# Optimization experiments

Measured on AMD Instinct MI355X. Metric: run time of the kernel, lower is better.

Reference implementation:

```python
import jax, jax.numpy as jnp
from jax import lax
import numpy as np

NUM_GROUP = 512   # num_group from __init__
GROUP_SIZE = 64   # group_size; walk length = GROUP_SIZE - 1


def setup_inputs() -> dict:
    key = jax.random.key(0)
    k1, k2, k3, k4 = jax.random.split(key, 4)
    B, N, V = 8, 65536, 32768
    xyz = jax.random.normal(k1, (B, N, 3), jnp.float32)
    ring_1 = jax.random.randint(k2, (B, N, 3), 0, N).astype(jnp.int32)
    vertices = jax.random.normal(k3, (B, V, 3), jnp.float32)
    faces = jax.random.randint(k4, (B, N, 3), 0, V).astype(jnp.int32)
    return {"xyz": xyz, "ring_1": ring_1, "vertices": vertices, "faces": faces}


def fps(xyz, num_group):
    # iterative farthest point sampling, deterministic start at index 0
    B, N, _ = xyz.shape
    idx0 = jnp.zeros((B,), jnp.int32)
    dist0 = jnp.full((B, N), 1e10, xyz.dtype)

    def body(carry, _):
        dist, last = carry
        p = jax.vmap(lambda x, i: x[i])(xyz, last)            # [B,3]
        d = jnp.sum((xyz - p[:, None, :]) ** 2, -1)           # [B,N]
        dist = jnp.minimum(dist, d)
        nxt = jnp.argmax(dist, axis=1).astype(jnp.int32)
        return (dist, nxt), nxt

    (_, _), rest = lax.scan(body, (dist0, idx0), None, length=num_group - 1)
    return jnp.concatenate([idx0[None, :], rest], 0).T        # [B,G]


def random_walks(ring, centers, n_faces, seq_len, key):
    # vectorized visited-mask random walk over all (batch, center) pairs
    B, G = centers.shape
    keys = jax.random.split(key, B * G).reshape(B, G)

    def one(nbrs_b, f0, k):
        visited = jnp.zeros((n_faces + 1,), bool).at[n_faces].set(True).at[f0].set(True)

        def step(carry, kk):
            cur, vis = carry
            nb = nbrs_b[cur]                                   # [3] neighbor ids
            mask = ~vis[nb]
            ka, kb = jax.random.split(kk)
            scores = jnp.where(mask, jax.random.uniform(ka, (3,)), -1.0)
            pick = nb[jnp.argmax(scores)]                      # random unvisited nbr
            rnd = jax.random.randint(kb, (), 0, n_faces)       # jump fallback
            nxt = jnp.where(mask.any(), pick, rnd).astype(jnp.int32)
            return (nxt, vis.at[nxt].set(True)), nxt

        (_, _), seq = lax.scan(step, (f0.astype(jnp.int32), visited),
                               jax.random.split(k, seq_len))
        return jnp.concatenate([f0[None].astype(jnp.int32), seq])

    return jax.vmap(lambda nb, cs, ks: jax.vmap(lambda f0, kk: one(nb, f0, kk))(cs, ks))(
        ring, centers, keys)                                   # [B,G,seq_len+1]


def reference(xyz, ring_1, vertices, faces):
    B, N, _ = xyz.shape
    center_idx = fps(xyz, NUM_GROUP)                           # [B,G]
    center = jax.vmap(lambda p, i: p[i])(xyz, center_idx)      # [B,G,3]
    idx = random_walks(ring_1, center_idx, N, GROUP_SIZE - 1, jax.random.key(42))
    neighborhood = jax.vmap(lambda p, i: p[i])(xyz, idx)       # [B,G,M,3]
    neighborhood = neighborhood - center[:, :, None, :]
    return neighborhood, center, idx.astype(jnp.int64)
```

## Files before the change

kernel.cpp:

```cpp
#include <hip/hip_runtime.h>
#include <stdint.h>

#define BB 8
#define NN 65536
#define GG 512
#define MM 64
#define STEPS 63
#define NWALK (BB*GG)

#define FPT 256
#define FPK 32
#define PPT (NN/(FPK*FPT))
#define FPS_BLOCKS (BB*FPK)

typedef unsigned long long ull;

__device__ __forceinline__ uint32_t rotl32(uint32_t x, uint32_t r){ return (x<<r)|(x>>(32u-r)); }

__device__ __forceinline__ void tf2x32(uint32_t k0, uint32_t k1, uint32_t x0, uint32_t x1,
                                       uint32_t &o0, uint32_t &o1){
  const uint32_t ks2 = k0 ^ k1 ^ 0x1BD11BDAu;
  x0 += k0; x1 += k1;
#define TFR(r) { x0 += x1; x1 = rotl32(x1,(r)); x1 ^= x0; }
  TFR(13) TFR(15) TFR(26) TFR(6)
  x0 += k1;  x1 += ks2 + 1u;
  TFR(17) TFR(29) TFR(16) TFR(24)
  x0 += ks2; x1 += k0 + 2u;
  TFR(13) TFR(15) TFR(26) TFR(6)
  x0 += k0;  x1 += k1 + 3u;
  TFR(17) TFR(29) TFR(16) TFR(24)
  x0 += k1;  x1 += ks2 + 4u;
  TFR(13) TFR(15) TFR(26) TFR(6)
  x0 += ks2; x1 += k0 + 5u;
#undef TFR
  o0 = x0; o1 = x1;
}

__global__ void rng_init_kernel(uint4* __restrict__ rng,
                                ull* __restrict__ slots,
                                int* __restrict__ center_idx){
  int tid = blockIdx.x*blockDim.x + threadIdx.x;
  if (tid < 2*BB*FPK) slots[tid] = 0ull;
  if (tid < BB) center_idx[tid*GG] = 0;
  if (tid >= STEPS*NWALK) return;
  int step = tid / NWALK;
  int walk = tid - step*NWALK;
  uint32_t kj0,kj1,t0,t1,a0,a1,b0,b1,p0,p1,q0,q1,r0,r1,l0,l1;
  tf2x32(0u, 42u, 0u, (uint32_t)walk, kj0, kj1);
  tf2x32(kj0, kj1, 0u, (uint32_t)step, t0, t1);
  tf2x32(t0, t1, 0u, 0u, a0, a1);
  tf2x32(t0, t1, 0u, 1u, b0, b1);
  tf2x32(a0, a1, 0u, 0u, p0, p1);
  tf2x32(a0, a1, 0u, 1u, q0, q1);
  tf2x32(a0, a1, 0u, 2u, r0, r1);
  tf2x32(b0, b1, 0u, 1u, l0, l1);
  uint4 e;
  e.x = ((p0 ^ p1) >> 9) | 0x3f800000u;
  e.y = ((q0 ^ q1) >> 9) | 0x3f800000u;
  e.z = ((r0 ^ r1) >> 9) | 0x3f800000u;
  e.w = (l0 ^ l1) & 0xFFFFu;
  rng[tid] = e;
}

__global__ __launch_bounds__(FPT) void fps_kernel(const float* __restrict__ xyz,
                                                  ull* __restrict__ slots,
                                                  int* __restrict__ center_idx){
  const int b = blockIdx.x & 7;
  const int k = blockIdx.x >> 3;
  const int t = threadIdx.x;
  const int w = t >> 6;
  const float* bx = xyz + (size_t)b*NN*3;
  float px[PPT], py[PPT], pz[PPT], dd[PPT];
  const int base = k*(FPT*PPT);
#pragma unroll
  for(int q=0;q<PPT;q++){
    int gi = base + q*FPT + t;
    px[q]=bx[3*gi]; py[q]=bx[3*gi+1]; pz[q]=bx[3*gi+2];
    dd[q]=1e10f;
  }
  __shared__ ull lred[FPT/64];
  __shared__ unsigned int bcw;
  __shared__ float bcx, bcy, bcz;
  float cx = bx[0], cy = bx[1], cz = bx[2];
  for(int it=1; it<GG; ++it){
    float bd = -1.0f; int bgi = 0;
#pragma unroll
    for(int q=0;q<PPT;q++){
      float dx = __fadd_rn(px[q], -cx);
      float dy = __fadd_rn(py[q], -cy);
      float dz = __fadd_rn(pz[q], -cz);
      float d  = __fmul_rn(dx,dx);
      d = __fadd_rn(d, __fmul_rn(dy,dy));
      d = __fadd_rn(d, __fmul_rn(dz,dz));
      float nd = fminf(dd[q], d);
      dd[q] = nd;
      int gi = base + q*FPT + t;
      if (nd > bd){ bd = nd; bgi = gi; }
    }
    ull best = ((ull)__float_as_uint(bd) << 32) | ((ull)(unsigned)(65535 - bgi) << 16);
#pragma unroll
    for(int off=32; off; off>>=1){
      ull o = __shfl_xor(best, off, 64);
      best = o > best ? o : best;
    }
    if ((t & 63)==0) lred[w] = best;
    __syncthreads();
    if (w==0){
      ull bb = lred[0];
#pragma unroll
      for(int j=1;j<FPT/64;j++){ ull o = lred[j]; bb = o>bb?o:bb; }
      ull* sl = slots + (((size_t)(it & 1))*BB + b)*FPK;
      if (t==0)
        __hip_atomic_store(&sl[k], bb | (unsigned)it, __ATOMIC_RELAXED, __HIP_MEMORY_SCOPE_AGENT);
      ull v = 0; float pcx=0.f, pcy=0.f, pcz=0.f;
      if (t < FPK){
        do { v = __hip_atomic_load(&sl[t], __ATOMIC_RELAXED, __HIP_MEMORY_SCOPE_AGENT); }
        while ((v & 0xFFFFull) != (ull)(unsigned)it);
        unsigned int idxj = 65535u - (unsigned)((v >> 16) & 0xFFFFu);
        pcx = bx[3*idxj]; pcy = bx[3*idxj+1]; pcz = bx[3*idxj+2];
      }
      ull m = v;
#pragma unroll
      for(int off=16; off; off>>=1){
        ull o = __shfl_xor(m, off, 64);
        m = o > m ? o : m;
      }
      ull bal = __ballot((t < FPK) && (v == m));
      int wl = (int)(__ffsll(bal) - 1);
      float wcx = __shfl(pcx, wl, 64);
      float wcy = __shfl(pcy, wl, 64);
      float wcz = __shfl(pcz, wl, 64);
      if (t==0){
        unsigned int widx = 65535u - (unsigned)((m >> 16) & 0xFFFFu);
        bcw = widx; bcx = wcx; bcy = wcy; bcz = wcz;
        if (k==0) center_idx[b*GG + it] = (int)widx;
      }
    }
    __syncthreads();
    cx = bcx; cy = bcy; cz = bcz;
  }
}

#define WBLK 64
__global__ __launch_bounds__(WBLK) void walk_kernel(const float* __restrict__ xyz,
                                                    const int* __restrict__ ring,
                                                    const uint4* __restrict__ rng,
                                                    const int* __restrict__ center_idx,
                                                    float* __restrict__ out){
  __shared__ uint32_t hashv[128*WBLK];
  const int t = threadIdx.x;
  for(int i=0;i<128;i++) hashv[i*WBLK + t] = 0u;

  const int walk = blockIdx.x*WBLK + t;
  const int b = walk >> 9;
  const float* bx = xyz + (size_t)b*NN*3;
  const int*  br = ring + (size_t)b*NN*3;

  float* out_nb = out;
  float* out_c  = out + (size_t)NWALK*MM*3;
  float* out_i  = out_c + (size_t)NWALK*3;

  const int cidx = center_idx[walk];
  const float cx = bx[3*cidx], cy = bx[3*cidx+1], cz = bx[3*cidx+2];
  out_c[walk*3+0]=cx; out_c[walk*3+1]=cy; out_c[walk*3+2]=cz;
  out_i[(size_t)walk*MM] = (float)cidx;
  { size_t o = (size_t)walk*MM*3; out_nb[o]=0.0f; out_nb[o+1]=0.0f; out_nb[o+2]=0.0f; }

  auto H = [](uint32_t v)->uint32_t { return (v*2654435761u) >> 25; };
  auto slow_has = [&](uint32_t v, uint32_t h)->bool{
    for(;;){ h=(h+1u)&127u; uint32_t c = hashv[h*WBLK+t];
             if (c==0u) return false;
             if (c==v+1u) return true; }
  };
  auto ins = [&](uint32_t v){
    uint32_t h = H(v);
    for(;;){ uint32_t c = hashv[h*WBLK+t];
             if (c==v+1u) return;
             if (c==0u){ hashv[h*WBLK+t]=v+1u; return; }
             h=(h+1u)&127u; }
  };

  ins((uint32_t)cidx);
  int n0 = br[3*cidx], n1 = br[3*cidx+1], n2 = br[3*cidx+2];
  int r00=br[3*n0], r01=br[3*n0+1], r02=br[3*n0+2];
  int r10=br[3*n1], r11=br[3*n1+1], r12=br[3*n1+2];
  int r20=br[3*n2], r21=br[3*n2+1], r22=br[3*n2+2];
  uint4 e = rng[walk];

  for(int i=0;i<STEPS;i++){
    uint4 en = (i < STEPS-1) ? rng[(size_t)(i+1)*NWALK + walk] : e;
    uint32_t h0=H((uint32_t)n0), h1=H((uint32_t)n1), h2=H((uint32_t)n2);
    uint32_t c0=hashv[h0*WBLK+t], c1=hashv[h1*WBLK+t], c2=hashv[h2*WBLK+t];
    bool v0 = (c0!=0u) && ((c0==(uint32_t)n0+1u) || slow_has((uint32_t)n0,h0));
    bool v1 = (c1!=0u) && ((c1==(uint32_t)n1+1u) || slow_has((uint32_t)n1,h1));
    bool v2 = (c2!=0u) && ((c2==(uint32_t)n2+1u) || slow_has((uint32_t)n2,h2));
    bool m0=!v0, m1=!v1, m2=!v2;
    float s0 = m0 ? __fadd_rn(__uint_as_float(e.x), -1.0f) : -1.0f;
    float s1 = m1 ? __fadd_rn(__uint_as_float(e.y), -1.0f) : -1.0f;
    float s2 = m2 ? __fadd_rn(__uint_as_float(e.z), -1.0f) : -1.0f;
    int s = 0; float sb = s0;
    if (s1 > sb){ sb=s1; s=1; }
    if (s2 > sb){ sb=s2; s=2; }
    bool any = m0|m1|m2;
    int pick = s==0 ? n0 : (s==1 ? n1 : n2);
    int nxt  = any ? pick : (int)e.w;
    if (any){
      uint32_t cs = s==0?c0:(s==1?c1:c2);
      uint32_t hs = s==0?h0:(s==1?h1:h2);
      if (cs==0u) hashv[hs*WBLK+t] = (uint32_t)nxt + 1u;
      else ins((uint32_t)nxt);
    } else {
      ins((uint32_t)nxt);
    }
    out_i[(size_t)walk*MM + i+1] = (float)nxt;
    float gx=bx[3*nxt], gy=bx[3*nxt+1], gz=bx[3*nxt+2];
    int nn0, nn1, nn2;
    if (any){
      nn0 = s==0?r00:(s==1?r10:r20);
      nn1 = s==0?r01:(s==1?r11:r21);
      nn2 = s==0?r02:(s==1?r12:r22);
    } else {
      nn0 = br[3*nxt]; nn1 = br[3*nxt+1]; nn2 = br[3*nxt+2];
    }
    n0=nn0; n1=nn1; n2=nn2;
    r00=br[3*n0]; r01=br[3*n0+1]; r02=br[3*n0+2];
    r10=br[3*n1]; r11=br[3*n1+1]; r12=br[3*n1+2];
    r20=br[3*n2]; r21=br[3*n2+1]; r22=br[3*n2+2];
    size_t o = ((size_t)walk*MM + (size_t)(i+1))*3;
    out_nb[o]   = __fadd_rn(gx, -cx);
    out_nb[o+1] = __fadd_rn(gy, -cy);
    out_nb[o+2] = __fadd_rn(gz, -cz);
    e = en;
  }
}

extern "C" void kernel_launch(void* const* d_in, const int* in_sizes, int n_in,
                              void* d_out, int out_size, void* d_ws, size_t ws_size,
                              hipStream_t stream) {
  const float* xyz  = (const float*)d_in[0];
  const int*   ring = (const int*)d_in[1];

  ull*   slots      = (ull*)d_ws;
  int*   center_idx = (int*)((char*)d_ws + 8192);
  uint4* rng        = (uint4*)((char*)d_ws + 8192 + 16384);
  float* out        = (float*)d_out;

  hipLaunchKernelGGL(rng_init_kernel, dim3((STEPS*NWALK)/256), dim3(256), 0, stream,
                     rng, slots, center_idx);
  hipLaunchKernelGGL(fps_kernel, dim3(FPS_BLOCKS), dim3(FPT), 0, stream,
                     xyz, slots, center_idx);
  hipLaunchKernelGGL(walk_kernel, dim3(NWALK/WBLK), dim3(WBLK), 0, stream,
                     xyz, ring, rng, center_idx, out);
}
```

Before: 1.540 ms.

## Replace FPS block-level reduction with per-wavefront global slot exchange

The FPS kernel no longer reduces inside each block through shared memory and __syncthreads. Each wavefront now publishes its candidate to a global slot array, then polls all 64 slots and reduces the winner itself. The block count per batch drops from 32 to 16, so each thread holds more points. This removes two block barriers per iteration, but every wavefront now spins on global atomics and reads more global data for each of the 511 sequential iterations.

```diff
diff --git a/kernel.cpp b/kernel.cpp
--- a/kernel.cpp
+++ b/kernel.cpp
@@ -9,7 +9,9 @@
 #define NWALK (BB*GG)
 
 #define FPT 256
-#define FPK 32
+#define FPK 16
+#define WPB (FPT/64)
+#define WVB (FPK*WPB)
 #define PPT (NN/(FPK*FPT))
 #define FPS_BLOCKS (BB*FPK)
 
@@ -40,7 +42,7 @@
                                 ull* __restrict__ slots,
                                 int* __restrict__ center_idx){
   int tid = blockIdx.x*blockDim.x + threadIdx.x;
-  if (tid < 2*BB*FPK) slots[tid] = 0ull;
+  if (tid < 2*BB*WVB) slots[tid] = 0ull;
   if (tid < BB) center_idx[tid*GG] = 0;
   if (tid >= STEPS*NWALK) return;
   int step = tid / NWALK;
@@ -66,21 +68,19 @@
                                                   ull* __restrict__ slots,
                                                   int* __restrict__ center_idx){
   const int b = blockIdx.x & 7;
-  const int k = blockIdx.x >> 3;
+  const int kblk = blockIdx.x >> 3;
   const int t = threadIdx.x;
-  const int w = t >> 6;
+  const int lane = t & 63;
+  const int wid = kblk*WPB + (t >> 6);
   const float* bx = xyz + (size_t)b*NN*3;
   float px[PPT], py[PPT], pz[PPT], dd[PPT];
-  const int base = k*(FPT*PPT);
+  const int base = kblk*(FPT*PPT);
 #pragma unroll
   for(int q=0;q<PPT;q++){
     int gi = base + q*FPT + t;
     px[q]=bx[3*gi]; py[q]=bx[3*gi+1]; pz[q]=bx[3*gi+2];
     dd[q]=1e10f;
   }
-  __shared__ ull lred[FPT/64];
-  __shared__ unsigned int bcw;
-  __shared__ float bcx, bcy, bcz;
   float cx = bx[0], cy = bx[1], cz = bx[2];
   for(int it=1; it<GG; ++it){
     float bd = -1.0f; int bgi = 0;
@@ -103,41 +103,29 @@
       ull o = __shfl_xor(best, off, 64);
       best = o > best ? o : best;
     }
-    if ((t & 63)==0) lred[w] = best;
-    __syncthreads();
-    if (w==0){
-      ull bb = lred[0];
-#pragma unroll
-      for(int j=1;j<FPT/64;j++){ ull o = lred[j]; bb = o>bb?o:bb; }
-      ull* sl = slots + (((size_t)(it & 1))*BB + b)*FPK;
-      if (t==0)
-        __hip_atomic_store(&sl[k], bb | (unsigned)it, __ATOMIC_RELAXED, __HIP_MEMORY_SCOPE_AGENT);
-      ull v = 0; float pcx=0.f, pcy=0.f, pcz=0.f;
-      if (t < FPK){
-        do { v = __hip_atomic_load(&sl[t], __ATOMIC_RELAXED, __HIP_MEMORY_SCOPE_AGENT); }
-        while ((v & 0xFFFFull) != (ull)(unsigned)it);
-        unsigned int idxj = 65535u - (unsigned)((v >> 16) & 0xFFFFu);
-        pcx = bx[3*idxj]; pcy = bx[3*idxj+1]; pcz = bx[3*idxj+2];
-      }
-      ull m = v;
-#pragma unroll
-      for(int off=16; off; off>>=1){
-        ull o = __shfl_xor(m, off, 64);
-        m = o > m ? o : m;
-      }
-      ull bal = __ballot((t < FPK) && (v == m));
-      int wl = (int)(__ffsll(bal) - 1);
-      float wcx = __shfl(pcx, wl, 64);
-      float wcy = __shfl(pcy, wl, 64);
-      float wcz = __shfl(pcz, wl, 64);
-      if (t==0){
-        unsigned int widx = 65535u - (unsigned)((m >> 16) & 0xFFFFu);
-        bcw = widx; bcx = wcx; bcy = wcy; bcz = wcz;
-        if (k==0) center_idx[b*GG + it] = (int)widx;
-      }
-    }
-    __syncthreads();
-    cx = bcx; cy = bcy; cz = bcz;
+    ull* sl = slots + (((size_t)(it & 1))*BB + b)*WVB;
+    if (lane==0)
+      __hip_atomic_store(&sl[wid], best | (unsigned)it, __ATOMIC_RELAXED, __HIP_MEMORY_SCOPE_AGENT);
+    ull v;
+    do { v = __hip_atomic_load(&sl[lane], __ATOMIC_RELAXED, __HIP_MEMORY_SCOPE_AGENT); }
+    while ((v & 0xFFFFull) != (ull)(unsigned)it);
+    unsigned int idxj = 65535u - (unsigned)((v >> 16) & 0xFFFFu);
+    float pcx = bx[3*idxj], pcy = bx[3*idxj+1], pcz = bx[3*idxj+2];
+    ull m = v;
+#pragma unroll
+    for(int off=32; off; off>>=1){
+      ull o = __shfl_xor(m, off, 64);
+      m = o > m ? o : m;
+    }
+    ull bal = __ballot(v == m);
+    int wl = (int)(__ffsll(bal) - 1);
+    cx = __shfl(pcx, wl, 64);
+    cy = __shfl(pcy, wl, 64);
+    cz = __shfl(pcz, wl, 64);
+    if (wid==0 && lane==0){
+      unsigned int widx = 65535u - (unsigned)((m >> 16) & 0xFFFFu);
+      __hip_atomic_store(&center_idx[b*GG + it], (int)widx, __ATOMIC_RELAXED, __HIP_MEMORY_SCOPE_AGENT);
+    }
   }
 }
 
```

Measured after the change: 2.679 ms. 74.0% more time.
